# Kernel tuning notes

Measured on AMD Instinct MI355X. Metric: run time of the kernel, lower is better.

The kernel has to match this reference:

```python
import jax, jax.numpy as jnp
import numpy as np

N_NODES = 100000
N_EDGES = 1600000
IN_FEATS = 128
OUT_FEATS = 48


def setup_inputs() -> dict:
    key = jax.random.key(0)
    ks = jax.random.split(key, 6)
    features = jax.random.normal(ks[0], (N_NODES, IN_FEATS), dtype=jnp.float32)
    # xavier_uniform for W.weight [out, in]
    lim_w = float(np.sqrt(6.0 / (IN_FEATS + OUT_FEATS)))
    W_w = jax.random.uniform(ks[1], (OUT_FEATS, IN_FEATS), dtype=jnp.float32, minval=-lim_w, maxval=lim_w)
    W_b = jnp.zeros((OUT_FEATS,), dtype=jnp.float32)
    # xavier_uniform for attn_w [2*out, 1]
    lim_a = float(np.sqrt(6.0 / (2 * OUT_FEATS + 1)))
    attn_w = jax.random.uniform(ks[2], (2 * OUT_FEATS, 1), dtype=jnp.float32, minval=-lim_a, maxval=lim_a)
    attn_b = jnp.zeros((1,), dtype=jnp.float32)
    src = jax.random.randint(ks[3], (N_EDGES,), 0, N_NODES, dtype=jnp.int32)
    dst = jax.random.randint(ks[4], (N_EDGES,), 0, N_NODES, dtype=jnp.int32)
    return {"features": features, "W_w": W_w, "W_b": W_b,
            "attn_w": attn_w, "attn_b": attn_b, "src": src, "dst": dst}


def reference(features, W_w, W_b, attn_w, attn_b, src, dst):
    n = features.shape[0]
    d = W_w.shape[0]
    # h = W(features)  [N, d]
    h = features @ W_w.T + W_b
    # cat([h[src], h[dst]]) @ attn_w == h[src] @ w_src + h[dst] @ w_dst
    w_src = attn_w[:d, 0]   # [d]
    w_dst = attn_w[d:, 0]   # [d]
    s_src = h @ w_src       # [N]
    s_dst = h @ w_dst       # [N]
    e = s_src[src] + s_dst[dst] + attn_b[0]            # [E]
    e = jax.nn.leaky_relu(e, negative_slope=0.2)
    # edge softmax grouped by destination node
    m = jax.ops.segment_max(e, dst, num_segments=n)     # [N]
    ex = jnp.exp(e - m[dst])                            # [E]
    denom = jax.ops.segment_sum(ex, dst, num_segments=n)  # [N]
    alpha = ex / denom[dst]                             # [E]
    # weighted scatter-sum: out[v] = sum_{(u,v) in E} alpha * h[u]
    msgs = h[src] * alpha[:, None]                      # [E, d]
    out = jax.ops.segment_sum(msgs, dst, num_segments=n)  # [N, d]
    return out
```

## Files before the change

kernel.cpp:

```cpp
#include <hip/hip_runtime.h>

#define NFEAT 128
#define DOUT 48
#define BSH 6
#define BNODES 64
#define PCAP 192
#define BCAP (PCAP * 8)
#define EPT 16
#define NBMAX 1568
#define HSTRIDE 32

typedef __attribute__((ext_vector_type(8))) short bf16x8;
typedef __attribute__((ext_vector_type(4))) float f32x4;

__device__ __forceinline__ float bf_lo(unsigned u) { return __uint_as_float(u << 16); }
__device__ __forceinline__ float bf_hi(unsigned u) { return __uint_as_float(u & 0xFFFF0000u); }
__device__ __forceinline__ unsigned bf_pack(float a, float b) {
    unsigned ua = __float_as_uint(a), ub = __float_as_uint(b);
    ua = (ua + 0x7FFFu + ((ua >> 16) & 1u)) >> 16;
    ub = (ub + 0x7FFFu + ((ub >> 16) & 1u)) & 0xFFFF0000u;
    return ua | ub;
}

__device__ __forceinline__ void split2(float x, short& hi, short& lo) {
    unsigned u = __float_as_uint(x);
    unsigned h = u & 0xFFFF0000u;
    hi = (short)(h >> 16);
    float r = x - __uint_as_float(h);
    unsigned v = __float_as_uint(r);
    lo = (short)((v + 0x7FFFu + ((v >> 16) & 1u)) >> 16);
}

__global__ __launch_bounds__(256) void k_proj(
    const float* __restrict__ feat, const float* __restrict__ Ww,
    const float* __restrict__ Wb, const float* __restrict__ attn_w,
    unsigned* __restrict__ hbf, float* __restrict__ s_src, float* __restrict__ s_dst,
    int n)
{
    __shared__ float hb[128][49];

    int tid  = threadIdx.x;
    int lane = tid & 63;
    int wv   = tid >> 6;
    int g    = lane >> 4;
    int r16  = lane & 15;

    int mbase = blockIdx.x * 128 + wv * 32;
    int na0 = mbase + r16;       if (na0 >= n) na0 = n - 1;
    int na1 = mbase + 16 + r16;  if (na1 >= n) na1 = n - 1;

    const float* fA0 = feat + (size_t)na0 * NFEAT + g * 4;
    const float* fA1 = feat + (size_t)na1 * NFEAT + g * 4;
    const float* wB  = Ww + (size_t)r16 * NFEAT + g * 4;

    f32x4 acc[2][3];
#pragma unroll
    for (int mt = 0; mt < 2; ++mt)
#pragma unroll
        for (int nt = 0; nt < 3; ++nt)
            acc[mt][nt] = (f32x4){0.f, 0.f, 0.f, 0.f};

#pragma unroll
    for (int ks = 0; ks < 4; ++ks) {
        f32x4 ra[4], rb[6];
        ra[0] = *(const f32x4*)(fA0 + ks * 32);
        ra[1] = *(const f32x4*)(fA0 + ks * 32 + 16);
        ra[2] = *(const f32x4*)(fA1 + ks * 32);
        ra[3] = *(const f32x4*)(fA1 + ks * 32 + 16);
        rb[0] = *(const f32x4*)(wB + ks * 32);
        rb[1] = *(const f32x4*)(wB + ks * 32 + 16);
        rb[2] = *(const f32x4*)(wB + 16 * NFEAT + ks * 32);
        rb[3] = *(const f32x4*)(wB + 16 * NFEAT + ks * 32 + 16);
        rb[4] = *(const f32x4*)(wB + 32 * NFEAT + ks * 32);
        rb[5] = *(const f32x4*)(wB + 32 * NFEAT + ks * 32 + 16);

        bf16x8 Ah[2], Al[2], Bh[3], Bl[3];
#pragma unroll
        for (int t = 0; t < 2; ++t) {
#pragma unroll
            for (int i = 0; i < 4; ++i) {
                short h, l;
                split2(ra[2 * t][i], h, l);     Ah[t][i] = h;     Al[t][i] = l;
                split2(ra[2 * t + 1][i], h, l); Ah[t][i + 4] = h; Al[t][i + 4] = l;
            }
        }
#pragma unroll
        for (int t = 0; t < 3; ++t) {
#pragma unroll
            for (int i = 0; i < 4; ++i) {
                short h, l;
                split2(rb[2 * t][i], h, l);     Bh[t][i] = h;     Bl[t][i] = l;
                split2(rb[2 * t + 1][i], h, l); Bh[t][i + 4] = h; Bl[t][i + 4] = l;
            }
        }
#pragma unroll
        for (int mt = 0; mt < 2; ++mt)
#pragma unroll
            for (int nt = 0; nt < 3; ++nt) {
                acc[mt][nt] = __builtin_amdgcn_mfma_f32_16x16x32_bf16(Ah[mt], Bh[nt], acc[mt][nt], 0, 0, 0);
                acc[mt][nt] = __builtin_amdgcn_mfma_f32_16x16x32_bf16(Al[mt], Bh[nt], acc[mt][nt], 0, 0, 0);
                acc[mt][nt] = __builtin_amdgcn_mfma_f32_16x16x32_bf16(Ah[mt], Bl[nt], acc[mt][nt], 0, 0, 0);
            }
    }

#pragma unroll
    for (int mt = 0; mt < 2; ++mt)
#pragma unroll
        for (int nt = 0; nt < 3; ++nt)
#pragma unroll
            for (int rr = 0; rr < 4; ++rr)
                hb[wv * 32 + mt * 16 + 4 * g + rr][nt * 16 + r16] = acc[mt][nt][rr];
    __syncthreads();

    int node = tid >> 1, part = tid & 1, jb = part * 24;
    int gn = blockIdx.x * 128 + node;
    float v[24];
    float ss = 0.f, sd = 0.f;
#pragma unroll
    for (int j = 0; j < 24; ++j) {
        float x = hb[node][jb + j] + Wb[jb + j];
        v[j] = x;
        ss = fmaf(x, attn_w[jb + j], ss);
        sd = fmaf(x, attn_w[DOUT + jb + j], sd);
    }
    ss += __shfl_xor(ss, 1, 64);
    sd += __shfl_xor(sd, 1, 64);

    if (gn < n) {
#pragma unroll
        for (int q = 0; q < 4; ++q) {
            int sub = part * 4 + q;
            uint4 u;
            u.x = bf_pack(v[6 * q + 0], v[6 * q + 1]);
            u.y = bf_pack(v[6 * q + 2], v[6 * q + 3]);
            u.z = bf_pack(v[6 * q + 4], v[6 * q + 5]);
            u.w = 0;
            *(uint4*)(hbf + (size_t)gn * HSTRIDE + sub * 4) = u;
        }
        if (part == 0) {
            s_src[gn] = ss;
            s_dst[gn] = sd;
        }
    }
}

__global__ __launch_bounds__(256) void k_bin(
    const int4* __restrict__ src4, const int4* __restrict__ dst4,
    const float* __restrict__ s_src, const float* __restrict__ s_dst,
    const float* __restrict__ attn_b,
    int* __restrict__ cursor, int2* __restrict__ ents, int nE, int NB)
{
    __shared__ int hist[NBMAX];
    __shared__ int bas[NBMAX];

    int tid = threadIdx.x;
    int cls = blockIdx.x & 7;
    long long e0 = (long long)blockIdx.x * 4096 + (long long)tid * EPT;

    for (int t = tid; t < NB; t += 256) hist[t] = 0;
    __syncthreads();

    int s[EPT], d[EPT];
    bool any = (e0 < nE);
#pragma unroll
    for (int q = 0; q < EPT / 4; ++q) {
        int4 sv = any ? src4[e0 / 4 + q] : make_int4(0, 0, 0, 0);
        int4 dv = any ? dst4[e0 / 4 + q] : make_int4(0, 0, 0, 0);
        s[4 * q + 0] = sv.x; s[4 * q + 1] = sv.y; s[4 * q + 2] = sv.z; s[4 * q + 3] = sv.w;
        d[4 * q + 0] = dv.x; d[4 * q + 1] = dv.y; d[4 * q + 2] = dv.z; d[4 * q + 3] = dv.w;
    }

    float vs[EPT], vd[EPT];
#pragma unroll
    for (int u = 0; u < EPT; ++u) vs[u] = s_src[s[u]];
#pragma unroll
    for (int u = 0; u < EPT; ++u) vd[u] = s_dst[d[u]];

    int rank[EPT];
#pragma unroll
    for (int u = 0; u < EPT; ++u)
        rank[u] = (e0 + u < nE) ? atomicAdd(&hist[d[u] >> BSH], 1) : 0;
    __syncthreads();

    for (int t = tid; t < NB; t += 256) {
        int c = hist[t];
        if (c > 0) bas[t] = atomicAdd(cursor + cls * NB + t, c);
    }
    __syncthreads();

    float ab = attn_b[0];
#pragma unroll
    for (int u = 0; u < EPT; ++u) {
        if (e0 + u < nE) {
            float v = vs[u] + vd[u] + ab;
            v = (v > 0.f) ? v : 0.2f * v;
            float x = __expf(v);
            int bkt = d[u] >> BSH;
            int slot = bas[bkt] + rank[u];
            if (slot < PCAP)
                ents[(size_t)bkt * BCAP + cls * PCAP + slot] =
                    make_int2(s[u] | ((d[u] & (BNODES - 1)) << 17), __float_as_int(x));
        }
    }
}

__global__ __launch_bounds__(256) void k_aggb(
    const unsigned* __restrict__ hbf, const int* __restrict__ cursor,
    const int2* __restrict__ ents, float* __restrict__ out, int n, int NB)
{
    __shared__ int2 se[BCAP];
    __shared__ unsigned short sidx[BCAP];
    __shared__ int c1[BNODES], c2[BNODES], lrp[BNODES + 1];
    __shared__ int cp[9];

    int b = blockIdx.x;
    int tid = threadIdx.x;
    const int2* ebase = ents + (size_t)b * BCAP;

    if (tid < BNODES) { c1[tid] = 0; c2[tid] = 0; }
    if (tid < 8) {
        int c = min(cursor[tid * NB + b], PCAP);
        int p = c;
#pragma unroll
        for (int o = 1; o < 8; o <<= 1) {
            int u = __shfl_up(p, o, 64);
            if (tid >= o) p += u;
        }
        cp[tid + 1] = p;
        if (tid == 0) cp[0] = 0;
    }
    __syncthreads();
    int total = cp[8];

#pragma unroll
    for (int c = 0; c < 8; ++c) {
        int s0 = cp[c], s1 = cp[c + 1];
        for (int i = s0 + tid; i < s1; i += 256) {
            int2 v = ebase[c * PCAP + (i - s0)];
            se[i] = v;
            atomicAdd(&c1[((unsigned)v.x) >> 17], 1);
        }
    }
    __syncthreads();

    if (tid < BNODES) {
        int v = c1[tid];
        int p = v;
#pragma unroll
        for (int o = 1; o < 64; o <<= 1) {
            int u = __shfl_up(p, o, 64);
            if (tid >= o) p += u;
        }
        lrp[tid] = p - v;
        if (tid == BNODES - 1) lrp[BNODES] = p;
    }
    __syncthreads();

    for (int i = tid; i < total; i += 256) {
        int dl = ((unsigned)se[i].x) >> 17;
        int pos = lrp[dl] + atomicAdd(&c2[dl], 1);
        sidx[pos] = (unsigned short)i;
    }
    __syncthreads();

    int grp = tid >> 3;
    int sub = tid & 7;
#pragma unroll
    for (int pass = 0; pass < 2; ++pass) {
        int dl = grp + pass * 32;
        int node = (b << BSH) + dl;
        bool live = (node < n);
        int st = lrp[dl];
        int en = live ? lrp[dl + 1] : st;
        float a0 = 0.f, a1 = 0.f, a2 = 0.f, a3 = 0.f, a4 = 0.f, a5 = 0.f, den = 0.f;
        int k = st;
        for (; k + 3 < en; k += 4) {
            int2 e0 = se[sidx[k]];
            int2 e1 = se[sidx[k + 1]];
            int2 e2 = se[sidx[k + 2]];
            int2 e3 = se[sidx[k + 3]];
            uint4 h0 = *(const uint4*)(hbf + (size_t)(e0.x & 0x1FFFF) * HSTRIDE + sub * 4);
            uint4 h1 = *(const uint4*)(hbf + (size_t)(e1.x & 0x1FFFF) * HSTRIDE + sub * 4);
            uint4 h2 = *(const uint4*)(hbf + (size_t)(e2.x & 0x1FFFF) * HSTRIDE + sub * 4);
            uint4 h3 = *(const uint4*)(hbf + (size_t)(e3.x & 0x1FFFF) * HSTRIDE + sub * 4);
            float x0 = __int_as_float(e0.y), x1 = __int_as_float(e1.y);
            float x2 = __int_as_float(e2.y), x3 = __int_as_float(e3.y);
            den += x0; den += x1; den += x2; den += x3;
            a0 = fmaf(x0, bf_lo(h0.x), a0); a1 = fmaf(x0, bf_hi(h0.x), a1);
            a2 = fmaf(x0, bf_lo(h0.y), a2); a3 = fmaf(x0, bf_hi(h0.y), a3);
            a4 = fmaf(x0, bf_lo(h0.z), a4); a5 = fmaf(x0, bf_hi(h0.z), a5);
            a0 = fmaf(x1, bf_lo(h1.x), a0); a1 = fmaf(x1, bf_hi(h1.x), a1);
            a2 = fmaf(x1, bf_lo(h1.y), a2); a3 = fmaf(x1, bf_hi(h1.y), a3);
            a4 = fmaf(x1, bf_lo(h1.z), a4); a5 = fmaf(x1, bf_hi(h1.z), a5);
            a0 = fmaf(x2, bf_lo(h2.x), a0); a1 = fmaf(x2, bf_hi(h2.x), a1);
            a2 = fmaf(x2, bf_lo(h2.y), a2); a3 = fmaf(x2, bf_hi(h2.y), a3);
            a4 = fmaf(x2, bf_lo(h2.z), a4); a5 = fmaf(x2, bf_hi(h2.z), a5);
            a0 = fmaf(x3, bf_lo(h3.x), a0); a1 = fmaf(x3, bf_hi(h3.x), a1);
            a2 = fmaf(x3, bf_lo(h3.y), a2); a3 = fmaf(x3, bf_hi(h3.y), a3);
            a4 = fmaf(x3, bf_lo(h3.z), a4); a5 = fmaf(x3, bf_hi(h3.z), a5);
        }
        for (; k < en; ++k) {
            int2 ed = se[sidx[k]];
            float x = __int_as_float(ed.y);
            den += x;
            uint4 h0 = *(const uint4*)(hbf + (size_t)(ed.x & 0x1FFFF) * HSTRIDE + sub * 4);
            a0 = fmaf(x, bf_lo(h0.x), a0); a1 = fmaf(x, bf_hi(h0.x), a1);
            a2 = fmaf(x, bf_lo(h0.y), a2); a3 = fmaf(x, bf_hi(h0.y), a3);
            a4 = fmaf(x, bf_lo(h0.z), a4); a5 = fmaf(x, bf_hi(h0.z), a5);
        }
        if (live) {
            float inv = (en > st) ? 1.f / den : 0.f;
            float* op = out + (size_t)node * DOUT + sub * 6;
            op[0] = a0 * inv;
            op[1] = a1 * inv;
            op[2] = a2 * inv;
            op[3] = a3 * inv;
            op[4] = a4 * inv;
            op[5] = a5 * inv;
        }
    }
}

extern "C" void kernel_launch(void* const* d_in, const int* in_sizes, int n_in,
                              void* d_out, int out_size, void* d_ws, size_t ws_size,
                              hipStream_t stream) {
    const float* feat   = (const float*)d_in[0];
    const float* Ww     = (const float*)d_in[1];
    const float* Wb     = (const float*)d_in[2];
    const float* attn_w = (const float*)d_in[3];
    const float* attn_b = (const float*)d_in[4];
    const int*   src    = (const int*)d_in[5];
    const int*   dst    = (const int*)d_in[6];

    int n  = in_sizes[0] / NFEAT;
    int nE = in_sizes[5];
    int NB = (n + BNODES - 1) / BNODES;
    int N8 = NB * 8;
    float* out = (float*)d_out;

    unsigned* hbf  = (unsigned*)d_ws;
    float* s_src   = (float*)(hbf + (size_t)n * HSTRIDE);
    float* s_dst   = s_src + n;
    int*   cursor  = (int*)(s_dst + n);
    int2*  ents    = (int2*)(cursor + N8);

    hipMemsetAsync(cursor, 0, (size_t)N8 * sizeof(int), stream);

    int NBp = (n + 127) / 128;
    k_proj<<<NBp, 256, 0, stream>>>(feat, Ww, Wb, attn_w, hbf, s_src, s_dst, n);
    int nbb = (nE + 4095) / 4096;
    k_bin<<<nbb, 256, 0, stream>>>((const int4*)src, (const int4*)dst,
                                   s_src, s_dst, attn_b, cursor, ents, nE, NB);
    k_aggb<<<NB, 256, 0, stream>>>(hbf, cursor, ents, out, n, NB);
}
```

Before: 181.4 us.

## Pre-split weights into bf16 hi/lo once and shrink edges per thread in binning

Adds a small kernel that splits the projection weights into packed bf16 hi/lo pairs once, so every k_proj block loads the packed pairs and skips the per-element split of W. Separately, k_bin now handles 4 edges per thread instead of 16, which launches four times as many blocks with fewer registers each. That should raise occupancy and latency hiding for the gathers. In exchange there is one extra kernel launch, and k_bin pays more per-block histogram init and more atomics traffic.

```diff
diff --git a/kernel.cpp b/kernel.cpp
--- a/kernel.cpp
+++ b/kernel.cpp
@@ -6,7 +6,7 @@
 #define BNODES 64
 #define PCAP 192
 #define BCAP (PCAP * 8)
-#define EPT 16
+#define EPT 4
 #define NBMAX 1568
 #define HSTRIDE 32
 
@@ -31,8 +31,19 @@
     lo = (short)((v + 0x7FFFu + ((v >> 16) & 1u)) >> 16);
 }
 
+__global__ __launch_bounds__(256) void k_wprep(
+    const float* __restrict__ Ww, unsigned* __restrict__ Whl)
+{
+    int i = blockIdx.x * 256 + threadIdx.x;
+    if (i < DOUT * NFEAT) {
+        short h, l;
+        split2(Ww[i], h, l);
+        Whl[i] = (unsigned)(unsigned short)h | ((unsigned)(unsigned short)l << 16);
+    }
+}
+
 __global__ __launch_bounds__(256) void k_proj(
-    const float* __restrict__ feat, const float* __restrict__ Ww,
+    const float* __restrict__ feat, const unsigned* __restrict__ Whl,
     const float* __restrict__ Wb, const float* __restrict__ attn_w,
     unsigned* __restrict__ hbf, float* __restrict__ s_src, float* __restrict__ s_dst,
     int n)
@@ -51,7 +62,7 @@
 
     const float* fA0 = feat + (size_t)na0 * NFEAT + g * 4;
     const float* fA1 = feat + (size_t)na1 * NFEAT + g * 4;
-    const float* wB  = Ww + (size_t)r16 * NFEAT + g * 4;
+    const unsigned* wB = Whl + (size_t)r16 * NFEAT + g * 4;
 
     f32x4 acc[2][3];
 #pragma unroll
@@ -62,17 +73,18 @@
 
 #pragma unroll
     for (int ks = 0; ks < 4; ++ks) {
-        f32x4 ra[4], rb[6];
+        f32x4 ra[4];
+        uint4 wb[6];
         ra[0] = *(const f32x4*)(fA0 + ks * 32);
         ra[1] = *(const f32x4*)(fA0 + ks * 32 + 16);
         ra[2] = *(const f32x4*)(fA1 + ks * 32);
         ra[3] = *(const f32x4*)(fA1 + ks * 32 + 16);
-        rb[0] = *(const f32x4*)(wB + ks * 32);
-        rb[1] = *(const f32x4*)(wB + ks * 32 + 16);
-        rb[2] = *(const f32x4*)(wB + 16 * NFEAT + ks * 32);
-        rb[3] = *(const f32x4*)(wB + 16 * NFEAT + ks * 32 + 16);
-        rb[4] = *(const f32x4*)(wB + 32 * NFEAT + ks * 32);
-        rb[5] = *(const f32x4*)(wB + 32 * NFEAT + ks * 32 + 16);
+        wb[0] = *(const uint4*)(wB + ks * 32);
+        wb[1] = *(const uint4*)(wB + ks * 32 + 16);
+        wb[2] = *(const uint4*)(wB + 16 * NFEAT + ks * 32);
+        wb[3] = *(const uint4*)(wB + 16 * NFEAT + ks * 32 + 16);
+        wb[4] = *(const uint4*)(wB + 32 * NFEAT + ks * 32);
+        wb[5] = *(const uint4*)(wB + 32 * NFEAT + ks * 32 + 16);
 
         bf16x8 Ah[2], Al[2], Bh[3], Bl[3];
 #pragma unroll
@@ -86,12 +98,16 @@
         }
 #pragma unroll
         for (int t = 0; t < 3; ++t) {
-#pragma unroll
-            for (int i = 0; i < 4; ++i) {
-                short h, l;
-                split2(rb[2 * t][i], h, l);     Bh[t][i] = h;     Bl[t][i] = l;
-                split2(rb[2 * t + 1][i], h, l); Bh[t][i + 4] = h; Bl[t][i + 4] = l;
-            }
+            unsigned w0 = wb[2 * t].x, w1 = wb[2 * t].y, w2 = wb[2 * t].z, w3 = wb[2 * t].w;
+            unsigned v0 = wb[2 * t + 1].x, v1 = wb[2 * t + 1].y, v2 = wb[2 * t + 1].z, v3 = wb[2 * t + 1].w;
+            Bh[t][0] = (short)(w0 & 0xFFFF); Bl[t][0] = (short)(w0 >> 16);
+            Bh[t][1] = (short)(w1 & 0xFFFF); Bl[t][1] = (short)(w1 >> 16);
+            Bh[t][2] = (short)(w2 & 0xFFFF); Bl[t][2] = (short)(w2 >> 16);
+            Bh[t][3] = (short)(w3 & 0xFFFF); Bl[t][3] = (short)(w3 >> 16);
+            Bh[t][4] = (short)(v0 & 0xFFFF); Bl[t][4] = (short)(v0 >> 16);
+            Bh[t][5] = (short)(v1 & 0xFFFF); Bl[t][5] = (short)(v1 >> 16);
+            Bh[t][6] = (short)(v2 & 0xFFFF); Bl[t][6] = (short)(v2 >> 16);
+            Bh[t][7] = (short)(v3 & 0xFFFF); Bl[t][7] = (short)(v3 >> 16);
         }
 #pragma unroll
         for (int mt = 0; mt < 2; ++mt)
@@ -155,7 +171,7 @@
 
     int tid = threadIdx.x;
     int cls = blockIdx.x & 7;
-    long long e0 = (long long)blockIdx.x * 4096 + (long long)tid * EPT;
+    long long e0 = (long long)blockIdx.x * (256 * EPT) + (long long)tid * EPT;
 
     for (int t = tid; t < NB; t += 256) hist[t] = 0;
     __syncthreads();
@@ -343,12 +359,14 @@
     float* s_dst   = s_src + n;
     int*   cursor  = (int*)(s_dst + n);
     int2*  ents    = (int2*)(cursor + N8);
+    unsigned* Whl  = (unsigned*)(ents + (size_t)NB * BCAP);
 
     hipMemsetAsync(cursor, 0, (size_t)N8 * sizeof(int), stream);
 
+    k_wprep<<<(DOUT * NFEAT + 255) / 256, 256, 0, stream>>>(Ww, Whl);
     int NBp = (n + 127) / 128;
-    k_proj<<<NBp, 256, 0, stream>>>(feat, Ww, Wb, attn_w, hbf, s_src, s_dst, n);
-    int nbb = (nE + 4095) / 4096;
+    k_proj<<<NBp, 256, 0, stream>>>(feat, Whl, Wb, attn_w, hbf, s_src, s_dst, n);
+    int nbb = (nE + 256 * EPT - 1) / (256 * EPT);
     k_bin<<<nbb, 256, 0, stream>>>((const int4*)src, (const int4*)dst,
                                    s_src, s_dst, attn_b, cursor, ents, nE, NB);
     k_aggb<<<NB, 256, 0, stream>>>(hbf, cursor, ents, out, n, NB);
```

Measured after the change: 188.9 us. +4.1%, slower.
